# Kernel tuning notes

Measured on AMD Instinct MI355X. Metric: run time of the kernel, lower is better.

## Reference

```python
import jax, jax.numpy as jnp
import numpy as np

B, L, D, H = 48, 512, 192, 6
DK = D // H
HID = 4 * D
EPS = 1e-5
SCALE = 1.0 / np.float32(np.sqrt(DK))


def _ln(x, g, b):
    mu = x.mean(-1, keepdims=True)
    v = ((x - mu) ** 2).mean(-1, keepdims=True)
    return (x - mu) * jax.lax.rsqrt(v + EPS) * g + b


def _mln(x, m, g, b):
    # masked layernorm: valid rows normalized, invalid rows pass through unchanged
    return jnp.where(m[..., None], _ln(x, g, b), x)


def _mha(q, k, v, mask, wq, bq, wk, bk, wv, bv, wo, bo):
    def proj(x, w, bb):
        return (x @ w + bb).reshape(B, L, H, DK).transpose(0, 2, 1, 3)  # [B,H,L,dk]
    Q, K, V = proj(q, wq, bq), proj(k, wk, bk), proj(v, wv, bv)
    s = jnp.einsum('bhqd,bhkd->bhqk', Q, K) * SCALE
    s = jnp.where(mask[:, None], -1e9, s)  # mask True = invalid pair
    p = jax.nn.softmax(s, axis=-1)
    o = jnp.einsum('bhqk,bhkd->bhqd', p, V).transpose(0, 2, 1, 3).reshape(B, L, D)
    return o @ wo + bo


def _forward(x_a, x_b, valid_a, valid_b,
             ln_a_g, ln_a_b, ln_b_g, ln_b_b, ln_oa_g, ln_oa_b, ln_ob_g, ln_ob_b,
             wq, bq, wk, bk, wv, bv, wo, bo,
             fln_g, fln_b, flno_g, flno_b, w1, b1, w2, b2):
    mB2A = ~(valid_a[:, :, None] & valid_b[:, None, :])  # [B,La,Lb]
    mA2B = ~(valid_b[:, :, None] & valid_a[:, None, :])
    a = _mln(x_a, valid_a, ln_a_g, ln_a_b)
    b = _mln(x_b, valid_b, ln_b_g, ln_b_b)
    oa = _mha(a, b, b, mB2A, wq, bq, wk, bk, wv, bv, wo, bo)
    oa = _mln(oa + x_a, valid_a, ln_oa_g, ln_oa_b)
    ob = _mha(b, a, a, mA2B, wq, bq, wk, bk, wv, bv, wo, bo)
    ob = _mln(ob + x_b, valid_b, ln_ob_g, ln_ob_b)

    def ffn(x, m):
        xn = _mln(x, m, fln_g, fln_b)
        y = jax.nn.gelu(xn @ w1 + b1, approximate=False) @ w2 + b2
        return _mln(x + y, m, flno_g, flno_b)

    return ffn(oa, valid_a), ffn(ob, valid_b)


def setup_inputs() -> dict:
    key = jax.random.key(0)
    ks = jax.random.split(key, 12)
    p = lambda k, s: jax.random.normal(k, s, dtype=jnp.float32) * 0.02
    ones = lambda s: jnp.ones(s, dtype=jnp.float32)
    zeros = lambda s: jnp.zeros(s, dtype=jnp.float32)
    return {
        'x_a': jax.random.normal(ks[0], (B, L, D), dtype=jnp.float32),
        'x_b': jax.random.normal(ks[1], (B, L, D), dtype=jnp.float32),
        'valid_a': jax.random.bernoulli(ks[2], 0.9, (B, L)),
        'valid_b': jax.random.bernoulli(ks[3], 0.9, (B, L)),
        'ln_a_g': ones((D,)), 'ln_a_b': zeros((D,)),
        'ln_b_g': ones((D,)), 'ln_b_b': zeros((D,)),
        'ln_oa_g': ones((D,)), 'ln_oa_b': zeros((D,)),
        'ln_ob_g': ones((D,)), 'ln_ob_b': zeros((D,)),
        'wq': p(ks[4], (D, D)), 'bq': zeros((D,)),
        'wk': p(ks[5], (D, D)), 'bk': zeros((D,)),
        'wv': p(ks[6], (D, D)), 'bv': zeros((D,)),
        'wo': p(ks[7], (D, D)), 'bo': zeros((D,)),
        'fln_g': ones((D,)), 'fln_b': zeros((D,)),
        'flno_g': ones((D,)), 'flno_b': zeros((D,)),
        'w1': p(ks[8], (D, HID)), 'b1': zeros((HID,)),
        'w2': p(ks[9], (HID, D)), 'b2': zeros((D,)),
    }


def reference(x_a, x_b, valid_a, valid_b,
              ln_a_g, ln_a_b, ln_b_g, ln_b_b, ln_oa_g, ln_oa_b, ln_ob_g, ln_ob_b,
              wq, bq, wk, bk, wv, bv, wo, bo,
              fln_g, fln_b, flno_g, flno_b, w1, b1, w2, b2):
    return _forward(x_a, x_b, valid_a, valid_b,
                    ln_a_g, ln_a_b, ln_b_g, ln_b_b, ln_oa_g, ln_oa_b, ln_ob_g, ln_ob_b,
                    wq, bq, wk, bk, wv, bv, wo, bo,
                    fln_g, fln_b, flno_g, flno_b, w1, b1, w2, b2)
```

## Files before the change

kernel.cpp:

```cpp
#include <hip/hip_runtime.h>
#include <math.h>

#define BB 48
#define LL 512
#define DD 192
#define HH 6
#define DKK 32
#define HID 768
#define ROWS (BB * LL)
#define BLD ((size_t)ROWS * DD)
#define SCALE_ATT 0.17677669529663687f
#define MASKED_S (-25.0f)

typedef unsigned short ushort_t;
typedef unsigned int uint_t;
typedef __bf16 bf16x8 __attribute__((ext_vector_type(8)));
typedef float f32x4 __attribute__((ext_vector_type(4)));

union U4BF8 { uint4 u; bf16x8 b; };

__device__ __forceinline__ ushort_t f2bf(float f) {
  union { float f; uint_t u; } v; v.f = f;
  uint_t r = v.u + 0x7fffu + ((v.u >> 16) & 1u);
  return (ushort_t)(r >> 16);
}
__device__ __forceinline__ float bf2f(ushort_t u) {
  union { uint_t u; float f; } v; v.u = ((uint_t)u) << 16; return v.f;
}

__device__ __forceinline__ int swz_w(int n, int k, int N) {
  return ((k >> 5) * (N >> 4) + (n >> 4)) * 512 +
         ((((k & 31) >> 3) << 4) + (n & 15)) * 8 + (k & 7);
}

__global__ __launch_bounds__(256) void pack_kernel(
    const float* __restrict__ wq, const float* __restrict__ wk,
    const float* __restrict__ wv, const float* __restrict__ wo,
    const float* __restrict__ w1, const float* __restrict__ w2,
    const float* __restrict__ bq, const float* __restrict__ bk,
    const float* __restrict__ bv,
    ushort_t* __restrict__ Wqkv, ushort_t* __restrict__ Wo,
    ushort_t* __restrict__ W1, ushort_t* __restrict__ W2,
    float* __restrict__ bqkv) {
  int i = blockIdx.x * 256 + threadIdx.x;
  if (i < 110592) {
    int n2 = i / 192, k = i - n2 * 192;
    int part = n2 / 192, n = n2 - part * 192;
    const float* src = part == 0 ? wq : (part == 1 ? wk : wv);
    Wqkv[swz_w(n2, k, 576)] = f2bf(src[k * 192 + n]);
  } else if (i < 147456) {
    int j = i - 110592;
    int n = j / 192, k = j - n * 192;
    Wo[swz_w(n, k, 192)] = f2bf(wo[k * 192 + n]);
  } else if (i < 294912) {
    int j = i - 147456;
    int n = j / 192, k = j - n * 192;
    W1[j] = f2bf(w1[k * 768 + n]);
  } else if (i < 442368) {
    int j = i - 294912;
    int n = j / 768, k = j - n * 768;
    W2[j] = f2bf(w2[k * 192 + n]);
  } else if (i < 442944) {
    int j = i - 442368;
    bqkv[j] = j < 192 ? bq[j] : (j < 384 ? bk[j - 192] : bv[j - 384]);
  }
}

__global__ __launch_bounds__(64) void mln2_kernel(
    const float* __restrict__ x0, const float* __restrict__ x1,
    const float* __restrict__ res0, const float* __restrict__ res1,
    const int* __restrict__ v0, const int* __restrict__ v1,
    const float* __restrict__ g0, const float* __restrict__ be0,
    const float* __restrict__ g1, const float* __restrict__ be1,
    float* __restrict__ outf, ushort_t* __restrict__ outb) {
  int row = blockIdx.x;
  int side = row >= ROWS;
  int r = side ? row - ROWS : row;
  int lane = threadIdx.x;
  const float* x = (side ? x1 : x0) + (size_t)r * DD;
  const float* rp = side ? res1 : res0;
  const float* g = side ? g1 : g0;
  const float* be = side ? be1 : be0;
  float v0_ = x[lane], v1_ = x[lane + 64], v2_ = x[lane + 128];
  if (rp != nullptr) {
    const float* rr = rp + (size_t)r * DD;
    v0_ += rr[lane]; v1_ += rr[lane + 64]; v2_ += rr[lane + 128];
  }
  float s = v0_ + v1_ + v2_;
#pragma unroll
  for (int off = 32; off; off >>= 1) s += __shfl_xor(s, off);
  float mu = s * (1.0f / 192.0f);
  float d0 = v0_ - mu, d1 = v1_ - mu, d2 = v2_ - mu;
  float ss = d0 * d0 + d1 * d1 + d2 * d2;
#pragma unroll
  for (int off = 32; off; off >>= 1) ss += __shfl_xor(ss, off);
  float inv = rsqrtf(ss * (1.0f / 192.0f) + 1e-5f);
  float r0, r1, r2;
  if ((side ? v1 : v0)[r]) {
    r0 = d0 * inv * g[lane]       + be[lane];
    r1 = d1 * inv * g[lane + 64]  + be[lane + 64];
    r2 = d2 * inv * g[lane + 128] + be[lane + 128];
  } else {
    r0 = v0_; r1 = v1_; r2 = v2_;
  }
  size_t o = (size_t)row * DD;
  if (outf != nullptr) {
    outf[o + lane] = r0; outf[o + lane + 64] = r1; outf[o + lane + 128] = r2;
  }
  if (outb != nullptr) {
    outb[o + lane] = f2bf(r0); outb[o + lane + 64] = f2bf(r1);
    outb[o + lane + 128] = f2bf(r2);
  }
}

__global__ __launch_bounds__(64) void mln_chain_kernel(
    const float* __restrict__ t,
    const float* __restrict__ res0, const float* __restrict__ res1,
    const int* __restrict__ v0, const int* __restrict__ v1,
    const float* __restrict__ g1a, const float* __restrict__ b1a,
    const float* __restrict__ g1b, const float* __restrict__ b1b,
    const float* __restrict__ g2, const float* __restrict__ b2,
    float* __restrict__ outf, ushort_t* __restrict__ outb) {
  int row = blockIdx.x;
  int side = row >= ROWS;
  int r = side ? row - ROWS : row;
  int lane = threadIdx.x;
  const float* tr = t + (size_t)row * DD;
  const float* rr = (side ? res1 : res0) + (size_t)r * DD;
  const float* g1 = side ? g1b : g1a;
  const float* b1 = side ? b1b : b1a;
  int vld = (side ? v1 : v0)[r];
  float v0_ = tr[lane] + rr[lane];
  float v1_ = tr[lane + 64] + rr[lane + 64];
  float v2_ = tr[lane + 128] + rr[lane + 128];
  float s = v0_ + v1_ + v2_;
#pragma unroll
  for (int off = 32; off; off >>= 1) s += __shfl_xor(s, off);
  float mu = s * (1.0f / 192.0f);
  float d0 = v0_ - mu, d1 = v1_ - mu, d2 = v2_ - mu;
  float ss = d0 * d0 + d1 * d1 + d2 * d2;
#pragma unroll
  for (int off = 32; off; off >>= 1) ss += __shfl_xor(ss, off);
  float inv = rsqrtf(ss * (1.0f / 192.0f) + 1e-5f);
  float y0, y1, y2;
  if (vld) {
    y0 = d0 * inv * g1[lane]       + b1[lane];
    y1 = d1 * inv * g1[lane + 64]  + b1[lane + 64];
    y2 = d2 * inv * g1[lane + 128] + b1[lane + 128];
  } else { y0 = v0_; y1 = v1_; y2 = v2_; }
  size_t o = (size_t)row * DD;
  outf[o + lane] = y0; outf[o + lane + 64] = y1; outf[o + lane + 128] = y2;
  float s2 = y0 + y1 + y2;
#pragma unroll
  for (int off = 32; off; off >>= 1) s2 += __shfl_xor(s2, off);
  float mu2 = s2 * (1.0f / 192.0f);
  float e0 = y0 - mu2, e1 = y1 - mu2, e2 = y2 - mu2;
  float ss2 = e0 * e0 + e1 * e1 + e2 * e2;
#pragma unroll
  for (int off = 32; off; off >>= 1) ss2 += __shfl_xor(ss2, off);
  float inv2 = rsqrtf(ss2 * (1.0f / 192.0f) + 1e-5f);
  float z0, z1, z2;
  if (vld) {
    z0 = e0 * inv2 * g2[lane]       + b2[lane];
    z1 = e1 * inv2 * g2[lane + 64]  + b2[lane + 64];
    z2 = e2 * inv2 * g2[lane + 128] + b2[lane + 128];
  } else { z0 = y0; z1 = y1; z2 = y2; }
  outb[o + lane] = f2bf(z0); outb[o + lane + 64] = f2bf(z1);
  outb[o + lane + 128] = f2bf(z2);
}

template <int NT, int F32OUT>
__global__ __launch_bounds__(256) void gemm_rowblk_kernel(
    const ushort_t* __restrict__ A, const ushort_t* __restrict__ Wsw,
    const float* __restrict__ bias, float* __restrict__ Cf,
    ushort_t* __restrict__ Cb) {
  constexpr int N = NT * 64;
  constexpr int CSB = N + 8;
  constexpr int CSF = N + 4;
  constexpr int AS_SH = 32 * 200;
  constexpr int CS_SH = F32OUT ? 32 * CSF * 2 : 32 * CSB;
  constexpr int SMEM_SH = AS_SH > CS_SH ? AS_SH : CS_SH;
  __shared__ ushort_t smem[SMEM_SH];
  ushort_t* As = smem;

  int tid = threadIdx.x;
  int w = tid >> 6, lane = tid & 63, l15 = lane & 15, kq = lane >> 4;
  int row0 = blockIdx.x * 32;

  {
    const ushort_t* ap = A + (size_t)row0 * 192;
#pragma unroll
    for (int i = 0; i < 3; ++i) {
      int idx = tid + i * 256;
      int r = idx / 24, c = (idx - r * 24) * 8;
      *(uint4*)(&As[r * 200 + c]) = *(const uint4*)(ap + idx * 8);
    }
  }
  __syncthreads();

  f32x4 acc[2][NT];
#pragma unroll
  for (int qs = 0; qs < 2; ++qs)
#pragma unroll
    for (int nt = 0; nt < NT; ++nt) acc[qs][nt] = (f32x4){0.f, 0.f, 0.f, 0.f};

#pragma unroll 1
  for (int kk = 0; kk < 6; ++kk) {
    bf16x8 af[2];
#pragma unroll
    for (int qs = 0; qs < 2; ++qs)
      af[qs] = *(const bf16x8*)(&As[(qs * 16 + l15) * 200 + kk * 32 + kq * 8]);
    const ushort_t* wp =
        Wsw + ((size_t)(kk * (N >> 4) + w * NT) << 9) + lane * 8;
#pragma unroll
    for (int nt = 0; nt < NT; ++nt) {
      U4BF8 wf;
      wf.u = *(const uint4*)(wp + (nt << 9));
#pragma unroll
      for (int qs = 0; qs < 2; ++qs)
        acc[qs][nt] = __builtin_amdgcn_mfma_f32_16x16x32_bf16(
            af[qs], wf.b, acc[qs][nt], 0, 0, 0);
    }
  }
  __syncthreads();

  if (!F32OUT) {
    ushort_t* Cs = smem;
#pragma unroll
    for (int nt = 0; nt < NT; ++nt) {
      int col = (w * NT + nt) * 16 + l15;
      float bb = bias[col];
#pragma unroll
      for (int qs = 0; qs < 2; ++qs)
#pragma unroll
        for (int r = 0; r < 4; ++r)
          Cs[(qs * 16 + kq * 4 + r) * CSB + col] = f2bf(acc[qs][nt][r] + bb);
    }
    __syncthreads();
    constexpr int UPR = (N * 2) / 16;
#pragma unroll
    for (int i = 0; i < (32 * UPR) / 256; ++i) {
      int idx = tid + i * 256;
      int r = idx / UPR, u = idx - r * UPR;
      *(uint4*)(Cb + (size_t)row0 * N + idx * 8) =
          *(const uint4*)(&Cs[r * CSB + u * 8]);
    }
  } else {
    float* Cs = (float*)smem;
#pragma unroll
    for (int nt = 0; nt < NT; ++nt) {
      int col = (w * NT + nt) * 16 + l15;
      float bb = bias[col];
#pragma unroll
      for (int qs = 0; qs < 2; ++qs)
#pragma unroll
        for (int r = 0; r < 4; ++r)
          Cs[(qs * 16 + kq * 4 + r) * CSF + col] = acc[qs][nt][r] + bb;
    }
    __syncthreads();
    constexpr int UPR = (N * 4) / 16;
#pragma unroll
    for (int i = 0; i < (32 * UPR) / 256; ++i) {
      int idx = tid + i * 256;
      int r = idx / UPR, u = idx - r * UPR;
      *(float4*)(Cf + (size_t)row0 * N + idx * 4) =
          *(const float4*)(&Cs[r * CSF + u * 4]);
    }
  }
}

__global__ __launch_bounds__(256, 3) void ffn_fused_kernel(
    const ushort_t* __restrict__ A, const ushort_t* __restrict__ W1t,
    const float* __restrict__ bias1, const ushort_t* __restrict__ W2t,
    const float* __restrict__ bias2, float* __restrict__ C) {
  __shared__ ushort_t As[64 * 200];
  __shared__ ushort_t Hs[2][64 * 72];
  int tid = threadIdx.x;
  int w = tid >> 6;
  int lane = tid & 63;
  int l15 = lane & 15;
  int kq = lane >> 4;
  int row0 = blockIdx.x * 64;

#pragma unroll
  for (int i = 0; i < 6; ++i) {
    int idx = tid + i * 256;
    int r = idx / 24, c = (idx % 24) * 8;
    *(uint4*)(&As[r * 200 + c]) = *(const uint4*)(A + (size_t)(row0 + r) * DD + c);
  }

  const ushort_t* w1p = W1t + (size_t)(w * 16 + l15) * DD + kq * 8;
  const ushort_t* w2p = W2t + (size_t)(w * 48 + l15) * HID + kq * 8;

  U4BF8 w1f[6], w1n[6], w2f[6];
#pragma unroll
  for (int kk = 0; kk < 6; ++kk)
    w1f[kk].u = *(const uint4*)(w1p + kk * 32);

  f32x4 Cacc[4][3];
#pragma unroll
  for (int qs = 0; qs < 4; ++qs)
#pragma unroll
    for (int nt = 0; nt < 3; ++nt) Cacc[qs][nt] = (f32x4){0.f, 0.f, 0.f, 0.f};

  __syncthreads();

  for (int hc = 0; hc < 12; ++hc) {
#pragma unroll
    for (int kk2 = 0; kk2 < 2; ++kk2)
#pragma unroll
      for (int nt = 0; nt < 3; ++nt)
        w2f[kk2 * 3 + nt].u =
            *(const uint4*)(w2p + (size_t)(nt * 16) * HID + hc * 64 + kk2 * 32);

    f32x4 Hacc[4];
#pragma unroll
    for (int qs = 0; qs < 4; ++qs) Hacc[qs] = (f32x4){0.f, 0.f, 0.f, 0.f};
#pragma unroll
    for (int kk = 0; kk < 6; ++kk) {
#pragma unroll
      for (int qs = 0; qs < 4; ++qs) {
        bf16x8 af = *(const bf16x8*)(&As[(qs * 16 + l15) * 200 + kk * 32 + kq * 8]);
        Hacc[qs] = __builtin_amdgcn_mfma_f32_16x16x32_bf16(
            af, w1f[kk].b, Hacc[qs], 0, 0, 0);
      }
    }

    if (hc < 11) {
#pragma unroll
      for (int kk = 0; kk < 6; ++kk)
        w1n[kk].u = *(const uint4*)(w1p + (size_t)(hc + 1) * 64 * DD + kk * 32);
    }

    {
      float bb = bias1[hc * 64 + w * 16 + l15];
      ushort_t* hb = &Hs[hc & 1][0];
#pragma unroll
      for (int qs = 0; qs < 4; ++qs)
#pragma unroll
        for (int r = 0; r < 4; ++r) {
          float x = Hacc[qs][r] + bb;
          x = 0.5f * x * (1.0f + erff(x * 0.70710678118654752f));
          hb[(qs * 16 + kq * 4 + r) * 72 + w * 16 + l15] = f2bf(x);
        }
    }
    __syncthreads();

#pragma unroll
    for (int kk2 = 0; kk2 < 2; ++kk2) {
      bf16x8 hf[4];
#pragma unroll
      for (int qs = 0; qs < 4; ++qs)
        hf[qs] = *(const bf16x8*)(&Hs[hc & 1][(qs * 16 + l15) * 72 + kk2 * 32 + kq * 8]);
#pragma unroll
      for (int nt = 0; nt < 3; ++nt)
#pragma unroll
        for (int qs = 0; qs < 4; ++qs)
          Cacc[qs][nt] = __builtin_amdgcn_mfma_f32_16x16x32_bf16(
              hf[qs], w2f[kk2 * 3 + nt].b, Cacc[qs][nt], 0, 0, 0);
    }

#pragma unroll
    for (int kk = 0; kk < 6; ++kk) w1f[kk] = w1n[kk];
  }

#pragma unroll
  for (int qs = 0; qs < 4; ++qs)
#pragma unroll
    for (int nt = 0; nt < 3; ++nt) {
      int col = w * 48 + nt * 16 + l15;
      float bb = bias2[col];
#pragma unroll
      for (int r = 0; r < 4; ++r) {
        int row = row0 + qs * 16 + kq * 4 + r;
        C[(size_t)row * DD + col] = Cacc[qs][nt][r] + bb;
      }
    }
}

__global__ __launch_bounds__(256) void attn_mfma_kernel(
    const ushort_t* __restrict__ QKV,
    const int* __restrict__ valid_a, const int* __restrict__ valid_b,
    ushort_t* __restrict__ out) {
  int i = blockIdx.x;
  int gid = ((i >> 5) << 3) | (i & 7);
  int qt = (i >> 3) & 3;
  int side = gid >= BB * HH;
  int grem = side ? gid - BB * HH : gid;
  int h = grem % HH;
  int batch = grem / HH;
  int tid = threadIdx.x;
  int w = tid >> 6;
  int lane = tid & 63;
  int l15 = lane & 15;
  int kq = lane >> 4;

  const int* validq = side ? valid_b : valid_a;
  const int* validk = side ? valid_a : valid_b;
  size_t qrow0  = (size_t)side * ROWS + (size_t)batch * LL;
  size_t kvrow0 = (size_t)(1 - side) * ROWS + (size_t)batch * LL;

  __shared__ ushort_t VsT[32 * 72];
  __shared__ ushort_t Ps[4][32 * 72];

  int qbase = qt * 128 + w * 32;

  U4BF8 qfrag[2];
#pragma unroll
  for (int qs = 0; qs < 2; ++qs)
    qfrag[qs].u = *(const uint4*)(QKV + (qrow0 + qbase + qs * 16 + l15) * 576 +
                                  h * DKK + kq * 8);

  int vq[2][4];
#pragma unroll
  for (int qs = 0; qs < 2; ++qs)
#pragma unroll
    for (int r = 0; r < 4; ++r)
      vq[qs][r] = validq[batch * LL + qbase + qs * 16 + kq * 4 + r];

  float lsum[2][4];
  f32x4 Oacc[2][2];
#pragma unroll
  for (int qs = 0; qs < 2; ++qs) {
#pragma unroll
    for (int r = 0; r < 4; ++r) lsum[qs][r] = 0.0f;
#pragma unroll
    for (int ds = 0; ds < 2; ++ds) Oacc[qs][ds] = (f32x4){0.f, 0.f, 0.f, 0.f};
  }

  for (int c = 0; c < LL; c += 64) {
    __syncthreads();
    uint4 vv = *(const uint4*)(QKV + (kvrow0 + c + lane) * 576 +
                               384 + h * DKK + w * 8);
    uint_t uu[4] = {vv.x, vv.y, vv.z, vv.w};
#pragma unroll
    for (int j = 0; j < 4; ++j) {
      VsT[(w * 8 + 2 * j) * 72 + lane]     = (ushort_t)(uu[j] & 0xffffu);
      VsT[(w * 8 + 2 * j + 1) * 72 + lane] = (ushort_t)(uu[j] >> 16);
    }
    __syncthreads();

    f32x4 S[2][4];
    int vk[4];
#pragma unroll
    for (int ks = 0; ks < 4; ++ks) {
      U4BF8 kf;
      kf.u = *(const uint4*)(QKV + (kvrow0 + c + ks * 16 + l15) * 576 +
                             192 + h * DKK + kq * 8);
      vk[ks] = validk[batch * LL + c + ks * 16 + l15];
#pragma unroll
      for (int qs = 0; qs < 2; ++qs) {
        f32x4 z = (f32x4){0.f, 0.f, 0.f, 0.f};
        S[qs][ks] = __builtin_amdgcn_mfma_f32_16x16x32_bf16(
            qfrag[qs].b, kf.b, z, 0, 0, 0);
      }
    }

#pragma unroll
    for (int qs = 0; qs < 2; ++qs)
#pragma unroll
      for (int ks = 0; ks < 4; ++ks)
#pragma unroll
        for (int r = 0; r < 4; ++r) {
          float x = (vq[qs][r] && vk[ks]) ? S[qs][ks][r] * SCALE_ATT : MASKED_S;
          float p = __expf(x);
          ushort_t pb = f2bf(p);
          lsum[qs][r] += bf2f(pb);
          Ps[w][(qs * 16 + kq * 4 + r) * 72 + ks * 16 + l15] = pb;
        }

#pragma unroll
    for (int kh = 0; kh < 2; ++kh) {
      bf16x8 pf[2], vf[2];
#pragma unroll
      for (int qs = 0; qs < 2; ++qs)
        pf[qs] = *(const bf16x8*)(&Ps[w][(qs * 16 + l15) * 72 + kh * 32 + kq * 8]);
#pragma unroll
      for (int ds = 0; ds < 2; ++ds)
        vf[ds] = *(const bf16x8*)(&VsT[(ds * 16 + l15) * 72 + kh * 32 + kq * 8]);
#pragma unroll
      for (int qs = 0; qs < 2; ++qs)
#pragma unroll
        for (int ds = 0; ds < 2; ++ds)
          Oacc[qs][ds] = __builtin_amdgcn_mfma_f32_16x16x32_bf16(
              pf[qs], vf[ds], Oacc[qs][ds], 0, 0, 0);
    }
  }

#pragma unroll
  for (int qs = 0; qs < 2; ++qs)
#pragma unroll
    for (int r = 0; r < 4; ++r) {
      float sm = lsum[qs][r];
#pragma unroll
      for (int off = 1; off < 16; off <<= 1) sm += __shfl_xor(sm, off);
      lsum[qs][r] = sm;
    }

#pragma unroll
  for (int qs = 0; qs < 2; ++qs)
#pragma unroll
    for (int ds = 0; ds < 2; ++ds)
#pragma unroll
      for (int r = 0; r < 4; ++r) {
        int q = qbase + qs * 16 + kq * 4 + r;
        out[(qrow0 + q) * DD + h * DKK + ds * 16 + l15] =
            f2bf(Oacc[qs][ds][r] / lsum[qs][r]);
      }
}

extern "C" void kernel_launch(void* const* d_in, const int* in_sizes, int n_in,
                              void* d_out, int out_size, void* d_ws, size_t ws_size,
                              hipStream_t stream) {
  const float* x_a = (const float*)d_in[0];
  const float* x_b = (const float*)d_in[1];
  const int* valid_a = (const int*)d_in[2];
  const int* valid_b = (const int*)d_in[3];
  const float* ln_a_g = (const float*)d_in[4];
  const float* ln_a_b = (const float*)d_in[5];
  const float* ln_b_g = (const float*)d_in[6];
  const float* ln_b_b = (const float*)d_in[7];
  const float* ln_oa_g = (const float*)d_in[8];
  const float* ln_oa_b = (const float*)d_in[9];
  const float* ln_ob_g = (const float*)d_in[10];
  const float* ln_ob_b = (const float*)d_in[11];
  const float* wq = (const float*)d_in[12];
  const float* bq = (const float*)d_in[13];
  const float* wk = (const float*)d_in[14];
  const float* bk = (const float*)d_in[15];
  const float* wv = (const float*)d_in[16];
  const float* bv = (const float*)d_in[17];
  const float* wo = (const float*)d_in[18];
  const float* bo = (const float*)d_in[19];
  const float* fln_g = (const float*)d_in[20];
  const float* fln_b = (const float*)d_in[21];
  const float* flno_g = (const float*)d_in[22];
  const float* flno_b = (const float*)d_in[23];
  const float* w1 = (const float*)d_in[24];
  const float* b1 = (const float*)d_in[25];
  const float* w2 = (const float*)d_in[26];
  const float* b2 = (const float*)d_in[27];

  char* wsb = (char*)d_ws;
  ushort_t* Wqkv = (ushort_t*)wsb;
  ushort_t* Wo_t = Wqkv + 110592;
  ushort_t* W1_t = Wo_t + 36864;
  ushort_t* W2_t = W1_t + 147456;
  float*    bqkv = (float*)(W2_t + 147456);
  ushort_t* lnFull = (ushort_t*)(wsb + 887040);
  ushort_t* attO   = lnFull;
  ushort_t* QKV = (ushort_t*)(wsb + 19761408);
  float* tmp = (float*)(wsb + 76384512);

  float* out_a = (float*)d_out;

  dim3 b64(64), b128(128), b256(256);
  dim3 gMln(2 * ROWS);
  dim3 gGemm(2 * ROWS / 32);
  dim3 gAttn(BB * HH * 4 * 2);
  dim3 gFFN(2 * ROWS / 64);

  hipLaunchKernelGGL(pack_kernel, dim3(1731), b256, 0, stream,
                     wq, wk, wv, wo, w1, w2, bq, bk, bv,
                     Wqkv, Wo_t, W1_t, W2_t, bqkv);

  hipLaunchKernelGGL(mln2_kernel, gMln, b64, 0, stream,
                     x_a, x_b, (const float*)nullptr, (const float*)nullptr,
                     valid_a, valid_b, ln_a_g, ln_a_b, ln_b_g, ln_b_b,
                     (float*)nullptr, lnFull);

  hipLaunchKernelGGL((gemm_rowblk_kernel<9, 0>), gGemm, b256, 0, stream,
                     lnFull, Wqkv, bqkv, (float*)nullptr, QKV);

  hipLaunchKernelGGL(attn_mfma_kernel, gAttn, b256, 0, stream,
                     QKV, valid_a, valid_b, attO);

  hipLaunchKernelGGL((gemm_rowblk_kernel<3, 1>), gGemm, b256, 0, stream,
                     attO, Wo_t, bo, tmp, (ushort_t*)nullptr);

  hipLaunchKernelGGL(mln_chain_kernel, gMln, b64, 0, stream,
                     tmp, x_a, x_b, valid_a, valid_b,
                     ln_oa_g, ln_oa_b, ln_ob_g, ln_ob_b, fln_g, fln_b,
                     out_a, lnFull);

  hipLaunchKernelGGL(ffn_fused_kernel, gFFN, b256, 0, stream,
                     lnFull, W1_t, b1, W2_t, b2, tmp);

  hipLaunchKernelGGL(mln2_kernel, gMln, b64, 0, stream,
                     tmp, tmp + BLD, out_a, out_a + BLD,
                     valid_a, valid_b, flno_g, flno_b, flno_g, flno_b,
                     out_a, (ushort_t*)nullptr);
}
```

Measured before the change: 357.8 us.

## Double-buffer V tile and prefetch next K/V chunk in attention loop

The attention kernel now double-buffers the transposed V tile in shared memory and prefetches the next chunk's K fragments, V row and key validity into registers while the current chunk computes. This removes one barrier per iteration and hides global-load latency. The softmax exponent is also rewritten as a single fma plus exp2 using a prescaled log2e factor and an additive mask bias, with native bf16 conversion. The row sum now accumulates the fp32 probability rather than the rounded bf16 value. The prefetching raises register pressure and may lower occupancy.

```diff
diff --git a/kernel.cpp b/kernel.cpp
--- a/kernel.cpp
+++ b/kernel.cpp
@@ -10,7 +10,8 @@
 #define ROWS (BB * LL)
 #define BLD ((size_t)ROWS * DD)
 #define SCALE_ATT 0.17677669529663687f
-#define MASKED_S (-25.0f)
+#define SB2 0.25503531f
+#define MASKED_X (-36.0f)
 
 typedef unsigned short ushort_t;
 typedef unsigned int uint_t;
@@ -18,6 +19,7 @@
 typedef float f32x4 __attribute__((ext_vector_type(4)));
 
 union U4BF8 { uint4 u; bf16x8 b; };
+union BFU { __bf16 h; ushort_t u; };
 
 __device__ __forceinline__ ushort_t f2bf(float f) {
   union { float f; uint_t u; } v; v.f = f;
@@ -26,6 +28,9 @@
 }
 __device__ __forceinline__ float bf2f(ushort_t u) {
   union { uint_t u; float f; } v; v.u = ((uint_t)u) << 16; return v.f;
+}
+__device__ __forceinline__ ushort_t cvt_bf(float f) {
+  BFU c; c.h = (__bf16)f; return c.u;
 }
 
 __device__ __forceinline__ int swz_w(int n, int k, int N) {
@@ -400,7 +405,7 @@
   size_t qrow0  = (size_t)side * ROWS + (size_t)batch * LL;
   size_t kvrow0 = (size_t)(1 - side) * ROWS + (size_t)batch * LL;
 
-  __shared__ ushort_t VsT[32 * 72];
+  __shared__ ushort_t VsT[2][32 * 72];
   __shared__ ushort_t Ps[4][32 * 72];
 
   int qbase = qt * 128 + w * 32;
@@ -411,12 +416,15 @@
     qfrag[qs].u = *(const uint4*)(QKV + (qrow0 + qbase + qs * 16 + l15) * 576 +
                                   h * DKK + kq * 8);
 
-  int vq[2][4];
+  float sqf[2][4], mq[2][4];
 #pragma unroll
   for (int qs = 0; qs < 2; ++qs)
 #pragma unroll
-    for (int r = 0; r < 4; ++r)
-      vq[qs][r] = validq[batch * LL + qbase + qs * 16 + kq * 4 + r];
+    for (int r = 0; r < 4; ++r) {
+      int vq = validq[batch * LL + qbase + qs * 16 + kq * 4 + r];
+      sqf[qs][r] = vq ? SB2 : 0.0f;
+      mq[qs][r]  = vq ? 0.0f : MASKED_X;
+    }
 
   float lsum[2][4];
   f32x4 Oacc[2][2];
@@ -428,32 +436,55 @@
     for (int ds = 0; ds < 2; ++ds) Oacc[qs][ds] = (f32x4){0.f, 0.f, 0.f, 0.f};
   }
 
+  uint4 vv = *(const uint4*)(QKV + (kvrow0 + lane) * 576 + 384 + h * DKK + w * 8);
+  U4BF8 kf[4];
+  int vki[4];
+#pragma unroll
+  for (int ks = 0; ks < 4; ++ks) {
+    kf[ks].u = *(const uint4*)(QKV + (kvrow0 + ks * 16 + l15) * 576 +
+                               192 + h * DKK + kq * 8);
+    vki[ks] = validk[batch * LL + ks * 16 + l15];
+  }
+
   for (int c = 0; c < LL; c += 64) {
+    int buf = (c >> 6) & 1;
+    {
+      uint_t uu[4] = {vv.x, vv.y, vv.z, vv.w};
+#pragma unroll
+      for (int j = 0; j < 4; ++j) {
+        VsT[buf][(w * 8 + 2 * j) * 72 + lane]     = (ushort_t)(uu[j] & 0xffffu);
+        VsT[buf][(w * 8 + 2 * j + 1) * 72 + lane] = (ushort_t)(uu[j] >> 16);
+      }
+    }
+    uint4 vvn;
+    if (c + 64 < LL)
+      vvn = *(const uint4*)(QKV + (kvrow0 + c + 64 + lane) * 576 +
+                            384 + h * DKK + w * 8);
     __syncthreads();
-    uint4 vv = *(const uint4*)(QKV + (kvrow0 + c + lane) * 576 +
-                               384 + h * DKK + w * 8);
-    uint_t uu[4] = {vv.x, vv.y, vv.z, vv.w};
-#pragma unroll
-    for (int j = 0; j < 4; ++j) {
-      VsT[(w * 8 + 2 * j) * 72 + lane]     = (ushort_t)(uu[j] & 0xffffu);
-      VsT[(w * 8 + 2 * j + 1) * 72 + lane] = (ushort_t)(uu[j] >> 16);
-    }
-    __syncthreads();
 
     f32x4 S[2][4];
-    int vk[4];
-#pragma unroll
-    for (int ks = 0; ks < 4; ++ks) {
-      U4BF8 kf;
-      kf.u = *(const uint4*)(QKV + (kvrow0 + c + ks * 16 + l15) * 576 +
-                             192 + h * DKK + kq * 8);
-      vk[ks] = validk[batch * LL + c + ks * 16 + l15];
+#pragma unroll
+    for (int ks = 0; ks < 4; ++ks)
 #pragma unroll
       for (int qs = 0; qs < 2; ++qs) {
         f32x4 z = (f32x4){0.f, 0.f, 0.f, 0.f};
         S[qs][ks] = __builtin_amdgcn_mfma_f32_16x16x32_bf16(
-            qfrag[qs].b, kf.b, z, 0, 0, 0);
+            qfrag[qs].b, kf[ks].b, z, 0, 0, 0);
       }
+
+    float mkb[4];
+#pragma unroll
+    for (int ks = 0; ks < 4; ++ks) mkb[ks] = vki[ks] ? 0.0f : MASKED_X;
+
+    U4BF8 kfn[4];
+    int vkn[4];
+    if (c + 64 < LL) {
+#pragma unroll
+      for (int ks = 0; ks < 4; ++ks) {
+        kfn[ks].u = *(const uint4*)(QKV + (kvrow0 + c + 64 + ks * 16 + l15) * 576 +
+                                    192 + h * DKK + kq * 8);
+        vkn[ks] = validk[batch * LL + c + 64 + ks * 16 + l15];
+      }
     }
 
 #pragma unroll
@@ -462,11 +493,10 @@
       for (int ks = 0; ks < 4; ++ks)
 #pragma unroll
         for (int r = 0; r < 4; ++r) {
-          float x = (vq[qs][r] && vk[ks]) ? S[qs][ks][r] * SCALE_ATT : MASKED_S;
-          float p = __expf(x);
-          ushort_t pb = f2bf(p);
-          lsum[qs][r] += bf2f(pb);
-          Ps[w][(qs * 16 + kq * 4 + r) * 72 + ks * 16 + l15] = pb;
+          float xs = fmaf(S[qs][ks][r], sqf[qs][r], fminf(mq[qs][r], mkb[ks]));
+          float p = __builtin_amdgcn_exp2f(xs);
+          lsum[qs][r] += p;
+          Ps[w][(qs * 16 + kq * 4 + r) * 72 + ks * 16 + l15] = cvt_bf(p);
         }
 
 #pragma unroll
@@ -477,7 +507,7 @@
         pf[qs] = *(const bf16x8*)(&Ps[w][(qs * 16 + l15) * 72 + kh * 32 + kq * 8]);
 #pragma unroll
       for (int ds = 0; ds < 2; ++ds)
-        vf[ds] = *(const bf16x8*)(&VsT[(ds * 16 + l15) * 72 + kh * 32 + kq * 8]);
+        vf[ds] = *(const bf16x8*)(&VsT[buf][(ds * 16 + l15) * 72 + kh * 32 + kq * 8]);
 #pragma unroll
       for (int qs = 0; qs < 2; ++qs)
 #pragma unroll
@@ -485,6 +515,10 @@
           Oacc[qs][ds] = __builtin_amdgcn_mfma_f32_16x16x32_bf16(
               pf[qs], vf[ds], Oacc[qs][ds], 0, 0, 0);
     }
+
+    vv = vvn;
+#pragma unroll
+    for (int ks = 0; ks < 4; ++ks) { kf[ks] = kfn[ks]; vki[ks] = vkn[ks]; }
   }
 
 #pragma unroll
```

Result: no change. 362.3 us (+1.2%).
